# Kernel optimization log

Measured on AMD Instinct MI355X. Metric: run time of the kernel, lower is better.

The kernel has to match this reference:

```python
import jax, jax.numpy as jnp
import numpy as np

HEADS = 8
DIM_HEAD = 64
SCALE = DIM_HEAD ** -0.5

def setup_inputs() -> dict:
    key = jax.random.key(0)
    k1, k2, k3 = jax.random.split(key, 3)
    B, N, D = 4, 2048, 512
    inner = HEADS * DIM_HEAD  # 512
    x = jax.random.normal(k1, (B, N, D), dtype=jnp.float32)
    w_qkv = jax.random.normal(k2, (D, inner * 3), dtype=jnp.float32) * (D ** -0.5)
    w_out = jax.random.normal(k3, (inner, D), dtype=jnp.float32) * (inner ** -0.5)
    b_out = jnp.zeros((D,), dtype=jnp.float32)
    return {"x": x, "w_qkv": w_qkv, "w_out": w_out, "b_out": b_out}

def reference(x, w_qkv, w_out, b_out):
    B, N, D = x.shape
    qkv = x @ w_qkv  # [B, N, 3*inner]
    q, k, v = jnp.split(qkv, 3, axis=-1)
    # b n (h d) -> b h n d
    def to_heads(t):
        return t.reshape(B, N, HEADS, DIM_HEAD).transpose(0, 2, 1, 3)
    q, k, v = to_heads(q), to_heads(k), to_heads(v)
    dots = jnp.einsum('bhid,bhjd->bhij', q, k) * SCALE  # [B,H,N,N]
    attn = jax.nn.softmax(dots, axis=-1)
    out = jnp.einsum('bhij,bhjd->bhid', attn, v)  # [B,H,N,Dh]
    out = out.transpose(0, 2, 1, 3).reshape(B, N, HEADS * DIM_HEAD)
    return out @ w_out + b_out
```

## Files before the change

kernel.cpp:

```cpp
#include <hip/hip_runtime.h>
#include <hip/hip_bf16.h>
#include <math.h>
#include <stdint.h>


typedef unsigned short u16;
typedef __attribute__((ext_vector_type(4))) float f32x4;
typedef __attribute__((ext_vector_type(8))) short bf16x8;
typedef __attribute__((ext_vector_type(4))) short s16x4;

#define AS1 __attribute__((address_space(1)))
#define AS3 __attribute__((address_space(3)))
#define MFMA(a, b, c) __builtin_amdgcn_mfma_f32_16x16x32_bf16(a, b, c, 0, 0, 0)
#define QSCALE 0.180336880f

__device__ __forceinline__ u16 f2bf(float f) {
  union { float f; unsigned u; } v; v.f = f;
  unsigned r = v.u + 0x7FFFu + ((v.u >> 16) & 1u);
  return (u16)(r >> 16);
}
__device__ __forceinline__ float bf2f(u16 b) {
  union { unsigned u; float f; } v; v.u = ((unsigned)b) << 16; return v.f;
}
__device__ __forceinline__ void splitbf(float x, u16& hi, u16& lo) {
  hi = f2bf(x); lo = f2bf(x - bf2f(hi));
}
__device__ __forceinline__ void gld16(const u16* g, u16* l) {
  __builtin_amdgcn_global_load_lds((const AS1 void*)g, (AS3 void*)l, 16, 0, 0);
}
__device__ __forceinline__ float u2f(unsigned u) {
  union { unsigned u; float f; } v; v.u = u; return v.f;
}
__device__ __forceinline__ unsigned f2u(float f) {
  union { float f; unsigned u; } v; v.f = f; return v.u;
}
__device__ __forceinline__ int cvtpk(float lo, float hi) {
  int r; asm("v_cvt_pk_bf16_f32 %0, %1, %2" : "=v"(r) : "v"(lo), "v"(hi));
  return r;
}
__device__ __forceinline__ float fexp2(float x) {
  float r; asm("v_exp_f32 %0, %1" : "=v"(r) : "v"(x));
  return r;
}

__global__ void k_cast(const float* __restrict__ s, u16* __restrict__ h, int n) {
  int i = (blockIdx.x * 256 + threadIdx.x) * 4;
  if (i < n) {
    f32x4 v = *(const f32x4*)&s[i];
    s16x4 hh;
    #pragma unroll
    for (int j = 0; j < 4; ++j) hh[j] = (short)f2bf(v[j]);
    *(s16x4*)&h[i] = hh;
  }
}

__global__ void k_tsplit(const float* __restrict__ s, u16* __restrict__ h,
                         u16* __restrict__ l, int N, int total) {
  int i = blockIdx.x * 256 + threadIdx.x;
  if (i < total) {
    int n = i >> 9, k = i & 511;
    u16 a, b; splitbf(s[(size_t)k * N + n], a, b);
    h[i] = a; l[i] = b;
  }
}

template <int TERMS>
__device__ __forceinline__ void gemm_core(
    const u16* __restrict__ Ah,
    const u16* __restrict__ Bh, const u16* __restrict__ Bl,
    char* sm, int rowA, int rowB, int tid, f32x4 (&acc)[4][4]) {
  const int wid = tid >> 6, lane = tid & 63;
  const int x = lane & 15, h = lane >> 4;
  const int wr = wid >> 1, wc = wid & 1;
  const int d0 = wid * 1024 + lane * 16;
  const int lg0 = d0 ^ (((d0 >> 7) & 7) << 4);
  const int srow = lg0 >> 6;
  const int scol = (lg0 & 63) >> 1;
  const int swk = ((lane >> 1) & 7) << 4;
  const char* smA = sm + (((wr * 64 + x) * 64 + h * 16) ^ swk);
  const char* smB = sm + (((wc * 64 + x) * 64 + h * 16) ^ swk);

  for (int kt = 0; kt < 16; ++kt) {
    const int kofs = kt * 32;
    __syncthreads();
    #pragma unroll
    for (int r = 0; r < 2; ++r) {
      const int row  = r * 64 + srow;
      const int ldst = r * 4096 + wid * 1024;
      const size_t ga = (size_t)(rowA + row) * 512 + kofs + scol;
      const size_t gb = (size_t)(rowB + row) * 512 + kofs + scol;
      gld16(Ah + ga, (u16*)(sm + ldst));
      gld16(Bh + gb, (u16*)(sm + 16384 + ldst));
      if (TERMS == 2) gld16(Bl + gb, (u16*)(sm + 24576 + ldst));
    }
    __syncthreads();
    bf16x8 a_h[4], b_h[4], b_l[4];
    #pragma unroll
    for (int i = 0; i < 4; ++i)
      a_h[i] = *(const bf16x8*)(smA + i * 1024);
    #pragma unroll
    for (int j = 0; j < 4; ++j) {
      b_h[j] = *(const bf16x8*)(smB + 16384 + j * 1024);
      if (TERMS == 2) b_l[j] = *(const bf16x8*)(smB + 24576 + j * 1024);
    }
    __builtin_amdgcn_s_setprio(1);
    #pragma unroll
    for (int i = 0; i < 4; ++i)
      #pragma unroll
      for (int j = 0; j < 4; ++j) {
        acc[i][j] = MFMA(a_h[i], b_h[j], acc[i][j]);
        if (TERMS == 2) acc[i][j] = MFMA(a_h[i], b_l[j], acc[i][j]);
      }
    __builtin_amdgcn_s_setprio(0);
  }
}

__global__ __launch_bounds__(256) void k_gemm_qkv(
    const u16* __restrict__ Ah,
    const u16* __restrict__ Bh, const u16* __restrict__ Bl,
    u16* __restrict__ Qb, u16* __restrict__ Kb, u16* __restrict__ Vt) {
  __shared__ __align__(1024) char sm[32768];
  const int tid = threadIdx.x, lane = tid & 63, wid = tid >> 6;
  const int x = lane & 15, h = lane >> 4;
  const int wr = wid >> 1, wc = wid & 1;
  const int rowA = blockIdx.x * 128, rowB = blockIdx.y * 128;
  f32x4 acc[4][4] = {};
  if (rowB >= 1024)
    gemm_core<1>(Ah, Bh, Bl, sm, rowA, rowB, tid, acc);
  else
    gemm_core<2>(Ah, Bh, Bl, sm, rowA, rowB, tid, acc);

  #pragma unroll
  for (int i = 0; i < 4; ++i)
    #pragma unroll
    for (int j = 0; j < 4; ++j) {
      const int n = rowB + wc * 64 + j * 16 + x;
      const int which = n >> 9;
      const int hh = (n >> 6) & 7, d = n & 63;
      const int m0 = rowA + wr * 64 + i * 16 + h * 4;
      const int b = m0 >> 11, is0 = m0 & 2047;
      if (which == 0) {
        #pragma unroll
        for (int r = 0; r < 4; ++r) {
          const size_t idx = ((size_t)((b * 8 + hh) * 2048 + is0 + r)) * 64 + d;
          Qb[idx] = f2bf(acc[i][j][r] * QSCALE);
        }
      } else if (which == 1) {
        #pragma unroll
        for (int r = 0; r < 4; ++r) {
          const size_t idx = ((size_t)((b * 8 + hh) * 2048 + is0 + r)) * 64 + d;
          Kb[idx] = f2bf(acc[i][j][r]);
        }
      } else {
        s16x4 vv;
        #pragma unroll
        for (int r = 0; r < 4; ++r) vv[r] = (short)f2bf(acc[i][j][r]);
        *(s16x4*)&Vt[((size_t)((b * 8 + hh) * 64 + d)) * 2048 + is0] = vv;
      }
    }
}

__global__ __launch_bounds__(256) void k_gemm_out(
    const u16* __restrict__ Ah, const u16* __restrict__ Bh,
    const float* __restrict__ bias, float* __restrict__ out) {
  __shared__ __align__(1024) char sm[32768];
  const int tid = threadIdx.x, lane = tid & 63, wid = tid >> 6;
  const int x = lane & 15, h = lane >> 4;
  const int wr = wid >> 1, wc = wid & 1;
  const int rowA = blockIdx.x * 128, rowB = blockIdx.y * 128;
  f32x4 acc[4][4] = {};
  gemm_core<1>(Ah, Bh, Bh, sm, rowA, rowB, tid, acc);

  #pragma unroll
  for (int i = 0; i < 4; ++i)
    #pragma unroll
    for (int j = 0; j < 4; ++j) {
      const int n = rowB + wc * 64 + j * 16 + x;
      #pragma unroll
      for (int r = 0; r < 4; ++r) {
        const int m = rowA + wr * 64 + i * 16 + h * 4 + r;
        out[(size_t)m * 512 + n] = acc[i][j][r] + bias[n];
      }
    }
}

__global__ __launch_bounds__(256, 3) void k_attn(
    const u16* __restrict__ Qb,
    const u16* __restrict__ Kb, const u16* __restrict__ Vt,
    u16* __restrict__ AO) {
  __shared__ __align__(1024) char sm[49152];
  const int tid = threadIdx.x, wid = tid >> 6, lane = tid & 63;
  const int x = lane & 15, h = lane >> 4;

  const int fid = blockIdx.x;
  const int l = (fid & 7) * 64 + (fid >> 3);
  const int qb = l & 15, bh = l >> 4;

  const size_t base = (size_t)bh * 2048 * 64;
  const int qr0 = qb * 128 + wid * 32;

  bf16x8 qh[2][2];
  #pragma unroll
  for (int g = 0; g < 2; ++g) {
    const size_t rq = base + (size_t)(qr0 + g * 16 + x) * 64 + h * 8;
    #pragma unroll
    for (int ks = 0; ks < 2; ++ks)
      qh[g][ks] = *(const bf16x8*)&Qb[rq + ks * 32];
  }

  bf16x8 ones;
  #pragma unroll
  for (int j = 0; j < 8; ++j) ones[j] = (short)0x3F80;

  const int db = tid * 16;
  const int lg = db ^ (((db >> 7) & 7) << 4);
  const int srow = lg >> 6;
  const int scb  = (lg & 63) >> 1;
  const size_t offK = (size_t)srow * 64 + scb;
  const size_t offV = (size_t)srow * 2048 + scb;

  const int swk = ((lane >> 1) & 7) << 4;
  const int rdo = (x * 64 + h * 16) ^ swk;
  char* const pb = sm + 32768 + wid * 4096;
  const int pxor = (x & 7) << 4;
  const int prow = x * 128;

  float mrun[2] = {-INFINITY, -INFINITY};
  f32x4 o[2][4] = {};
  f32x4 os[2] = {};

  {
    gld16(Kb + base + offK,      (u16*)(sm + db));
    gld16(Kb + base + offK + 32, (u16*)(sm + 4096 + db));
    gld16(Vt + base + offV,      (u16*)(sm + 8192 + db));
    gld16(Vt + base + offV + 32, (u16*)(sm + 12288 + db));
  }

  for (int kv = 0; kv < 32; ++kv) {
    const int bb = (kv & 1) * 16384;
    __builtin_amdgcn_s_barrier();
    if (kv < 31) {
      const size_t kvb = (size_t)(kv + 1) * 64;
      char* buf = sm + (16384 - bb);
      gld16(Kb + base + kvb * 64 + offK,      (u16*)(buf + db));
      gld16(Kb + base + kvb * 64 + offK + 32, (u16*)(buf + 4096 + db));
      gld16(Vt + base + kvb + offV,           (u16*)(buf + 8192 + db));
      gld16(Vt + base + kvb + offV + 32,      (u16*)(buf + 12288 + db));
      asm volatile("s_waitcnt vmcnt(4)" ::: "memory");
    } else {
      asm volatile("s_waitcnt vmcnt(0)" ::: "memory");
    }
    __builtin_amdgcn_s_barrier();

    const char* smb = sm + bb + rdo;

    f32x4 s[2][4] = {};
    __builtin_amdgcn_s_setprio(1);
    #pragma unroll
    for (int c = 0; c < 4; ++c)
      #pragma unroll
      for (int ks = 0; ks < 2; ++ks) {
        bf16x8 kb_ = *(const bf16x8*)(smb + ks * 4096 + c * 1024);
        s[0][c] = MFMA(kb_, qh[0][ks], s[0][c]);
        s[1][c] = MFMA(kb_, qh[1][ks], s[1][c]);
      }
    __builtin_amdgcn_s_setprio(0);

    float pm[2];
    #pragma unroll
    for (int g = 0; g < 2; ++g) {
      float m0 = fmaxf(fmaxf(s[g][0][0], s[g][0][1]), s[g][0][2]);
      float m1 = fmaxf(fmaxf(s[g][0][3], s[g][1][0]), s[g][1][1]);
      float m2 = fmaxf(fmaxf(s[g][1][2], s[g][1][3]), s[g][2][0]);
      float m3 = fmaxf(fmaxf(s[g][2][1], s[g][2][2]), s[g][2][3]);
      float m4 = fmaxf(fmaxf(s[g][3][0], s[g][3][1]), s[g][3][2]);
      float m5 = fmaxf(fmaxf(m0, m1), m2);
      float p  = fmaxf(fmaxf(fmaxf(m3, m4), s[g][3][3]), m5);
      p = fmaxf(p, __shfl_xor(p, 16, 64));
      p = fmaxf(p, __shfl_xor(p, 32, 64));
      pm[g] = p;
    }

    if (__any((pm[0] > mrun[0] + 7.0f) || (pm[1] > mrun[1] + 7.0f))) {
      #pragma unroll
      for (int g = 0; g < 2; ++g) {
        float mnew = fmaxf(mrun[g], pm[g]);
        float scl = fexp2(mrun[g] - mnew);
        mrun[g] = mnew;
        #pragma unroll
        for (int r = 0; r < 4; ++r) {
          float sq = u2f((unsigned)__builtin_amdgcn_ds_bpermute(
              (20 * h + r) * 4, (int)f2u(scl)));
          os[g][r] *= sq;
          #pragma unroll
          for (int dg = 0; dg < 4; ++dg) o[g][dg][r] *= sq;
        }
      }
    }

    #pragma unroll
    for (int g = 0; g < 2; ++g)
      #pragma unroll
      for (int c = 0; c < 4; ++c) {
        int w0 = cvtpk(fexp2(s[g][c][0] - mrun[g]),
                       fexp2(s[g][c][1] - mrun[g]));
        int w1 = cvtpk(fexp2(s[g][c][2] - mrun[g]),
                       fexp2(s[g][c][3] - mrun[g]));
        int* dst = (int*)(pb + g * 2048 + prow + ((c * 32 + h * 8) ^ pxor));
        dst[0] = w0; dst[1] = w1;
      }

    __builtin_amdgcn_s_setprio(1);
    #pragma unroll
    for (int ch = 0; ch < 2; ++ch) {
      bf16x8 pa0 = *(const bf16x8*)(pb + prow +
                                    ((ch * 64 + h * 16) ^ pxor));
      bf16x8 pa1 = *(const bf16x8*)(pb + 2048 + prow +
                                    ((ch * 64 + h * 16) ^ pxor));
      os[0] = MFMA(pa0, ones, os[0]);
      os[1] = MFMA(pa1, ones, os[1]);
      #pragma unroll
      for (int dg = 0; dg < 4; ++dg) {
        bf16x8 vb = *(const bf16x8*)(smb + 8192 + ch * 4096 + dg * 1024);
        o[0][dg] = MFMA(pa0, vb, o[0][dg]);
        o[1][dg] = MFMA(pa1, vb, o[1][dg]);
      }
    }
    __builtin_amdgcn_s_setprio(0);
  }

  const int b_ = bh >> 3, head = bh & 7;
  #pragma unroll
  for (int g = 0; g < 2; ++g)
    #pragma unroll
    for (int r = 0; r < 4; ++r) {
      const float inv = 1.0f / os[g][r];
      const int row = qr0 + g * 16 + h * 4 + r;
      #pragma unroll
      for (int dg = 0; dg < 4; ++dg) {
        AO[((size_t)(b_ * 2048 + row)) * 512 + head * 64 + dg * 16 + x] =
            f2bf(o[g][dg][r] * inv);
      }
    }
}

extern "C" void kernel_launch(void* const* d_in, const int* in_sizes, int n_in,
                              void* d_out, int out_size, void* d_ws, size_t ws_size,
                              hipStream_t stream) {
  const float* x    = (const float*)d_in[0];
  const float* wqkv = (const float*)d_in[1];
  const float* wout = (const float*)d_in[2];
  const float* bout = (const float*)d_in[3];
  float* out = (float*)d_out;

  char* w = (char*)d_ws;
  u16* xh  = (u16*)(w + 0);
  u16* wqh = (u16*)(w + 16777216);
  u16* wql = (u16*)(w + 18350080);
  u16* woh = (u16*)(w + 19922944);
  u16* wol = (u16*)(w + 20447232);
  u16* Qb  = (u16*)(w + 20971520);
  u16* Kb  = (u16*)(w + 37748736);
  u16* Vt  = (u16*)(w + 46137344);
  u16* AO  = (u16*)(w + 54525952);

  k_cast  <<<4096, 256, 0, stream>>>(x, xh, 4194304);
  k_tsplit<<<3072, 256, 0, stream>>>(wqkv, wqh, wql, 1536, 786432);
  k_tsplit<<<1024, 256, 0, stream>>>(wout, woh, wol, 512, 262144);
  k_gemm_qkv<<<dim3(64, 12), 256, 0, stream>>>(xh, wqh, wql, Qb, Kb, Vt);
  k_attn<<<512, 256, 0, stream>>>(Qb, Kb, Vt, AO);
  k_gemm_out<<<dim3(64, 4), 256, 0, stream>>>(AO, woh, bout, out);
}
```

Before: 107.1 us.

## Split attention KV range across two blocks and merge partials in a combine kernel

Each attention block now handles half of the 2048 keys, which doubles the grid from 512 to 1024 blocks. Every block writes unnormalized fp32 partial outputs plus its per-row running max and sum. A new combine kernel rescales and merges the two halves, normalizes, and writes the bf16 attention output. The aim is fuller use of the CUs and the available occupancy during attention, at the cost of extra global traffic for the fp32 partials and one additional kernel launch.

```diff
diff --git a/kernel.cpp b/kernel.cpp
--- a/kernel.cpp
+++ b/kernel.cpp
@@ -187,17 +187,20 @@
 __global__ __launch_bounds__(256, 3) void k_attn(
     const u16* __restrict__ Qb,
     const u16* __restrict__ Kb, const u16* __restrict__ Vt,
-    u16* __restrict__ AO) {
+    float* __restrict__ OP,
+    float* __restrict__ Mm,
+    float* __restrict__ Sm) {
   __shared__ __align__(1024) char sm[49152];
   const int tid = threadIdx.x, wid = tid >> 6, lane = tid & 63;
   const int x = lane & 15, h = lane >> 4;
 
   const int fid = blockIdx.x;
-  const int l = (fid & 7) * 64 + (fid >> 3);
-  const int qb = l & 15, bh = l >> 4;
+  const int l = (fid & 7) * 128 + (fid >> 3);
+  const int half = l & 1, qb = (l >> 1) & 15, bh = l >> 5;
 
   const size_t base = (size_t)bh * 2048 * 64;
   const int qr0 = qb * 128 + wid * 32;
+  const int kt0 = half * 16;
 
   bf16x8 qh[2][2];
   #pragma unroll
@@ -230,17 +233,19 @@
   f32x4 os[2] = {};
 
   {
-    gld16(Kb + base + offK,      (u16*)(sm + db));
-    gld16(Kb + base + offK + 32, (u16*)(sm + 4096 + db));
-    gld16(Vt + base + offV,      (u16*)(sm + 8192 + db));
-    gld16(Vt + base + offV + 32, (u16*)(sm + 12288 + db));
-  }
-
-  for (int kv = 0; kv < 32; ++kv) {
+    const size_t kB = base + (size_t)kt0 * 64 * 64;
+    const size_t vB = base + (size_t)kt0 * 64;
+    gld16(Kb + kB + offK,      (u16*)(sm + db));
+    gld16(Kb + kB + offK + 32, (u16*)(sm + 4096 + db));
+    gld16(Vt + vB + offV,      (u16*)(sm + 8192 + db));
+    gld16(Vt + vB + offV + 32, (u16*)(sm + 12288 + db));
+  }
+
+  for (int kv = 0; kv < 16; ++kv) {
     const int bb = (kv & 1) * 16384;
     __builtin_amdgcn_s_barrier();
-    if (kv < 31) {
-      const size_t kvb = (size_t)(kv + 1) * 64;
+    if (kv < 15) {
+      const size_t kvb = (size_t)(kt0 + kv + 1) * 64;
       char* buf = sm + (16384 - bb);
       gld16(Kb + base + kvb * 64 + offK,      (u16*)(buf + db));
       gld16(Kb + base + kvb * 64 + offK + 32, (u16*)(buf + 4096 + db));
@@ -329,19 +334,44 @@
     __builtin_amdgcn_s_setprio(0);
   }
 
-  const int b_ = bh >> 3, head = bh & 7;
-  #pragma unroll
-  for (int g = 0; g < 2; ++g)
+  float* op = OP + (size_t)half * 15728640 +
+              ((size_t)(bh * 2048 + qr0)) * 64;
+  #pragma unroll
+  for (int g = 0; g < 2; ++g) {
     #pragma unroll
     for (int r = 0; r < 4; ++r) {
-      const float inv = 1.0f / os[g][r];
-      const int row = qr0 + g * 16 + h * 4 + r;
-      #pragma unroll
-      for (int dg = 0; dg < 4; ++dg) {
-        AO[((size_t)(b_ * 2048 + row)) * 512 + head * 64 + dg * 16 + x] =
-            f2bf(o[g][dg][r] * inv);
-      }
-    }
+      const int row = g * 16 + h * 4 + r;
+      #pragma unroll
+      for (int dg = 0; dg < 4; ++dg)
+        op[(size_t)row * 64 + dg * 16 + x] = o[g][dg][r];
+      if (x == 0)
+        Sm[half * 65536 + bh * 2048 + qr0 + g * 16 + h * 4 + r] = os[g][r];
+    }
+    if (h == 0)
+      Mm[half * 65536 + bh * 2048 + qr0 + g * 16 + x] = mrun[g];
+  }
+}
+
+__global__ __launch_bounds__(256) void k_combine(
+    const float* __restrict__ OP, const float* __restrict__ Mm,
+    const float* __restrict__ Sm, u16* __restrict__ AO) {
+  const int gi = blockIdx.x * 256 + threadIdx.x;
+  const int d4 = (gi & 15) * 4;
+  const int rb = gi >> 4;
+  const float m1 = Mm[rb], m2 = Mm[65536 + rb];
+  const float s1 = Sm[rb], s2 = Sm[65536 + rb];
+  const float m = fmaxf(m1, m2);
+  const float a1 = fexp2(m1 - m), a2 = fexp2(m2 - m);
+  const float inv = 1.0f / (s1 * a1 + s2 * a2);
+  const float w1 = a1 * inv, w2 = a2 * inv;
+  f32x4 o1 = *(const f32x4*)&OP[(size_t)rb * 64 + d4];
+  f32x4 o2 = *(const f32x4*)&OP[15728640 + (size_t)rb * 64 + d4];
+  const int bh = rb >> 11, row = rb & 2047;
+  const int b = bh >> 3, head = bh & 7;
+  s16x4 r_;
+  #pragma unroll
+  for (int j = 0; j < 4; ++j) r_[j] = (short)f2bf(o1[j] * w1 + o2[j] * w2);
+  *(s16x4*)&AO[((size_t)(b * 2048 + row)) * 512 + head * 64 + d4] = r_;
 }
 
 extern "C" void kernel_launch(void* const* d_in, const int* in_sizes, int n_in,
@@ -363,11 +393,15 @@
   u16* Kb  = (u16*)(w + 37748736);
   u16* Vt  = (u16*)(w + 46137344);
   u16* AO  = (u16*)(w + 54525952);
+  float* OP = (float*)(w + 0);
+  float* Mm = (float*)(w + 16777216);
+  float* Sm = (float*)(w + 17301504);
 
   k_cast  <<<4096, 256, 0, stream>>>(x, xh, 4194304);
   k_tsplit<<<3072, 256, 0, stream>>>(wqkv, wqh, wql, 1536, 786432);
   k_tsplit<<<1024, 256, 0, stream>>>(wout, woh, wol, 512, 262144);
   k_gemm_qkv<<<dim3(64, 12), 256, 0, stream>>>(xh, wqh, wql, Qb, Kb, Vt);
-  k_attn<<<512, 256, 0, stream>>>(Qb, Kb, Vt, AO);
+  k_attn<<<1024, 256, 0, stream>>>(Qb, Kb, Vt, OP, Mm, Sm);
+  k_combine<<<4096, 256, 0, stream>>>(OP, Mm, Sm, AO);
   k_gemm_out<<<dim3(64, 4), 256, 0, stream>>>(AO, woh, bout, out);
 }
```

After: 114.5 us. 6.9% more time.
